# Kernel optimization log

Hardware: AMD Instinct MI355X
Metric: run time of the kernel (lower is better)

Reference implementation:

```python
import jax, jax.numpy as jnp
import numpy as np

D_IN = 512
D_OUT = 512
CONTEXT_LEN = 4096


def setup_inputs() -> dict:
    key = jax.random.key(0)
    kx, kq, kk, kv = jax.random.split(key, 4)
    x = jax.random.normal(kx, (4, 4096, D_IN), dtype=jnp.float32)
    # nn.Linear weights: shape (d_out, d_in), y = x @ W.T (no bias, qkv_bias=False)
    s = 1.0 / np.sqrt(D_IN)
    w_q = jax.random.uniform(kq, (D_OUT, D_IN), dtype=jnp.float32, minval=-s, maxval=s)
    w_k = jax.random.uniform(kk, (D_OUT, D_IN), dtype=jnp.float32, minval=-s, maxval=s)
    w_v = jax.random.uniform(kv, (D_OUT, D_IN), dtype=jnp.float32, minval=-s, maxval=s)
    return {"x": x, "w_q": w_q, "w_k": w_k, "w_v": w_v}


def reference(x, w_q, w_k, w_v):
    b, n, _ = x.shape
    q = jnp.einsum('bnd,od->bno', x, w_q)
    k = jnp.einsum('bnd,od->bno', x, w_k)
    v = jnp.einsum('bnd,od->bno', x, w_v)
    scores = jnp.einsum('bqo,bko->bqk', q, k)  # [b, n, n]
    # Faithful to source: mask buffer is triu(zeros) -> all-False, masked_fill is a no-op.
    mask = jnp.triu(jnp.zeros((CONTEXT_LEN, CONTEXT_LEN), dtype=jnp.float32), k=1).astype(bool)[:n, :n]
    scores = jnp.where(mask, -jnp.inf, scores)
    attn = jax.nn.softmax(scores / np.sqrt(D_OUT).astype(np.float32), axis=-1)
    # dropout rate 0.0 (eval/reference) -> identity
    return jnp.einsum('bqk,bko->bqo', attn, v)
```

## Files before the change

### kernel.cpp

```cpp
#include <hip/hip_runtime.h>
#include <math.h>

typedef __attribute__((ext_vector_type(8))) __bf16 bf16x8;
typedef __attribute__((ext_vector_type(8))) short  short8;
typedef __attribute__((ext_vector_type(4))) unsigned short ushort4v;
typedef __attribute__((ext_vector_type(4))) float  floatx4;

typedef __attribute__((address_space(1))) unsigned int as1_u32;
typedef __attribute__((address_space(3))) unsigned int as3_u32;

__device__ __forceinline__ void async_copy16(const void* g, void* l) {
  __builtin_amdgcn_global_load_lds((const as1_u32*)g, (as3_u32*)l, 16, 0, 0);
}

__device__ __forceinline__ unsigned short f2bf(float f) {
  union { float f; unsigned u; } v; v.f = f;
  unsigned r = v.u + 0x7fffu + ((v.u >> 16) & 1u);
  return (unsigned short)(r >> 16);
}

__device__ __forceinline__ floatx4 mfma_bf16(bf16x8 a, bf16x8 b, floatx4 c) {
  return __builtin_amdgcn_mfma_f32_16x16x32_bf16(a, b, c, 0, 0, 0);
}

__device__ __forceinline__ bf16x8 lds_frag(const unsigned short* p) {
  return *(const bf16x8*)(const void*)p;
}

__global__ __launch_bounds__(256)
void prep(const float* __restrict__ x,  const float* __restrict__ wq,
          const float* __restrict__ wk, const float* __restrict__ wv,
          unsigned short* __restrict__ Xb, unsigned short* __restrict__ Wqb,
          unsigned short* __restrict__ Wkb, unsigned short* __restrict__ Wvb) {
  const int i = blockIdx.x * 256 + threadIdx.x;
  const float* s; unsigned short* d; int off;
  if (i < 2097152)             { s = x;  d = Xb;  off = i; }
  else if (i < 2097152+65536)  { s = wq; d = Wqb; off = i - 2097152; }
  else if (i < 2097152+131072) { s = wk; d = Wkb; off = i - (2097152+65536); }
  else                         { s = wv; d = Wvb; off = i - (2097152+131072); }
  const float4 v = ((const float4*)s)[off];
  ushort4v o;
  o.x = f2bf(v.x); o.y = f2bf(v.y); o.z = f2bf(v.z); o.w = f2bf(v.w);
  *(ushort4v*)(void*)(d + (size_t)off * 4) = o;
}

__global__ __launch_bounds__(256, 2)
void gemm_qkv(const unsigned short* __restrict__ Xb,
              const unsigned short* __restrict__ Wqb,
              const unsigned short* __restrict__ Wkb,
              const unsigned short* __restrict__ Wvb,
              unsigned short* __restrict__ Q,
              unsigned short* __restrict__ K,
              unsigned short* __restrict__ Vt) {
  const int gid = blockIdx.x;
  const unsigned short *A, *B; unsigned short* C;
  int m0, n0, N;
  if (gid < 512) {
    A = Xb; B = Wqb; C = Q; N = 512;
    m0 = (gid & 127) * 128; n0 = (gid >> 7) * 128;
  } else if (gid < 1024) {
    A = Xb; B = Wkb; C = K; N = 512;
    m0 = ((gid - 512) & 127) * 128; n0 = ((gid - 512) >> 7) * 128;
  } else {
    A = Wvb; B = Xb; C = Vt; N = 16384;
    m0 = ((gid - 1024) & 3) * 128; n0 = ((gid - 1024) >> 2) * 128;
  }

  __shared__ unsigned short As[128 * 64];
  __shared__ unsigned short Bs[128 * 64];
  const int tid = threadIdx.x;
  const int w = tid >> 6, lane = tid & 63;
  const int quad = lane >> 4, l15 = lane & 15;
  const int wm = w >> 1, wn = w & 1;
  const int row_l = lane >> 3;
  const int chk   = lane & 7;
  const int s_chk = chk ^ row_l;

  floatx4 acc[16];
#pragma unroll
  for (int i = 0; i < 16; i++) acc[i] = (floatx4){0.f, 0.f, 0.f, 0.f};

  for (int kt = 0; kt < 8; kt++) {
    __syncthreads();
#pragma unroll
    for (int i = 0; i < 4; i++) {
      const int c = w * 4 + i;
      const int row = c * 8 + row_l;
      async_copy16(A + (size_t)(m0 + row) * 512 + kt * 64 + s_chk * 8, &As[c * 512]);
      async_copy16(B + (size_t)(n0 + row) * 512 + kt * 64 + s_chk * 8, &Bs[c * 512]);
    }
    __syncthreads();
#pragma unroll
    for (int kc = 0; kc < 2; kc++) {
      bf16x8 af[4], bfv[4];
#pragma unroll
      for (int i = 0; i < 4; i++) {
        const int pc = ((kc * 4 + quad) ^ (l15 & 7)) * 8;
        af[i]  = lds_frag(&As[(wm * 64 + i * 16 + l15) * 64 + pc]);
        bfv[i] = lds_frag(&Bs[(wn * 64 + i * 16 + l15) * 64 + pc]);
      }
#pragma unroll
      for (int mi = 0; mi < 4; mi++)
#pragma unroll
        for (int ni = 0; ni < 4; ni++)
          acc[mi * 4 + ni] = mfma_bf16(af[mi], bfv[ni], acc[mi * 4 + ni]);
    }
  }
#pragma unroll
  for (int mi = 0; mi < 4; mi++)
#pragma unroll
    for (int ni = 0; ni < 4; ni++)
#pragma unroll
      for (int r = 0; r < 4; r++) {
        const int row = m0 + wm * 64 + mi * 16 + quad * 4 + r;
        const int col = n0 + wn * 64 + ni * 16 + l15;
        C[(size_t)row * N + col] = f2bf(acc[mi * 4 + ni][r]);
      }
}

#define SCALE 0.044194173824159216f

__global__ __launch_bounds__(512, 2)
void attn_kernel(const unsigned short* __restrict__ Qg,
                 const unsigned short* __restrict__ Kg,
                 const unsigned short* __restrict__ Vt,
                 float* __restrict__ O) {
  __shared__ unsigned short Ks[64 * 512];
  __shared__ unsigned short Vs[512 * 64];
  __shared__ float Sx[64][65];
  __shared__ unsigned short Pb[64 * 72];
  __shared__ float m_row[64], l_row[64], a_row[64];

  const int tid = threadIdx.x;
  const int w = tid >> 6, lane = tid & 63;
  const int quad = lane >> 4, l15 = lane & 15;
  const int wq = w >> 1, wd = w & 1;

  const int g0 = blockIdx.x;
  const int g  = (g0 & 7) * 32 + (g0 >> 3);
  const int b  = g >> 6;
  const int q0 = (g & 63) * 64;

  if (tid < 64) { m_row[tid] = -3.0e38f; l_row[tid] = 0.f; }

  bf16x8 qf[16];
  {
    const unsigned short* qrow = Qg + (size_t)(b * 4096 + q0 + wq * 16 + l15) * 512;
#pragma unroll
    for (int i = 0; i < 16; i++)
      qf[i] = *(const bf16x8*)(const void*)(qrow + i * 32 + quad * 8);
  }

  floatx4 oacc[16];
#pragma unroll
  for (int i = 0; i < 16; i++) oacc[i] = (floatx4){0.f, 0.f, 0.f, 0.f};

  const unsigned short* kb0 = Kg + (size_t)b * 4096 * 512;
  const unsigned short* vb0 = Vt + (size_t)b * 4096;
  const int v_d = lane >> 3, v_schk = (lane & 7) ^ v_d;

  auto issue_K = [&](int kt_) {
#pragma unroll
    for (int u = 0; u < 8; u++) {
      const int row = w * 8 + u;
      async_copy16(kb0 + ((size_t)kt_ * 64 + row) * 512 + (lane ^ u) * 8,
                   &Ks[row * 512]);
    }
  };
  auto issue_V = [&](int kt_) {
#pragma unroll
    for (int u = 0; u < 8; u++) {
      const int d = w * 64 + u * 8 + v_d;
      async_copy16(vb0 + (size_t)kt_ * 64 + (size_t)d * 16384 + v_schk * 8,
                   &Vs[(w * 64 + u * 8) * 64]);
    }
  };

  const int srow = tid >> 3, sg = tid & 7;

  issue_K(0);

  for (int kt = 0; kt < 64; kt++) {
    asm volatile("s_waitcnt vmcnt(0)" ::: "memory");
    __builtin_amdgcn_sched_barrier(0);
    __syncthreads();
    issue_V(kt);

    floatx4 sacc[2];
    sacc[0] = (floatx4){0.f, 0.f, 0.f, 0.f};
    sacc[1] = (floatx4){0.f, 0.f, 0.f, 0.f};
#pragma unroll
    for (int kk = 0; kk < 16; kk++) {
#pragma unroll
      for (int s = 0; s < 2; s++) {
        const int krow = wd * 32 + s * 16 + l15;
        bf16x8 bfr = lds_frag(&Ks[krow * 512 + (((kk * 4 + quad) ^ (l15 & 7)) * 8)]);
        sacc[s] = mfma_bf16(qf[kk], bfr, sacc[s]);
      }
    }
#pragma unroll
    for (int s = 0; s < 2; s++)
#pragma unroll
      for (int r = 0; r < 4; r++)
        Sx[wq * 16 + quad * 4 + r][wd * 32 + s * 16 + l15] = sacc[s][r] * SCALE;
    __syncthreads();

    {
      float vals[8];
      float tmax = -3.0e38f;
#pragma unroll
      for (int j = 0; j < 8; j++) {
        float xv = Sx[srow][sg * 8 + j];
        xv = fminf(fmaxf(xv, -1.0e4f), 1.0e4f);
        vals[j] = xv;
        tmax = fmaxf(tmax, xv);
      }
      tmax = fmaxf(tmax, __shfl_xor(tmax, 1));
      tmax = fmaxf(tmax, __shfl_xor(tmax, 2));
      tmax = fmaxf(tmax, __shfl_xor(tmax, 4));
      const float m_old = m_row[srow];
      const float m_new = fmaxf(m_old, tmax);
      const float alpha = __expf(m_old - m_new);
      float lsum = 0.f;
      short8 pvec;
#pragma unroll
      for (int j = 0; j < 8; j++) {
        const float p = __expf(vals[j] - m_new);
        lsum += p;
        pvec[j] = (short)f2bf(p);
      }
      lsum += __shfl_xor(lsum, 1);
      lsum += __shfl_xor(lsum, 2);
      lsum += __shfl_xor(lsum, 4);
      *(short8*)(void*)&Pb[srow * 72 + sg * 8] = pvec;
      if (sg == 0) {
        m_row[srow] = m_new;
        l_row[srow] = l_row[srow] * alpha + lsum;
        a_row[srow] = alpha;
      }
    }
    __syncthreads();

    float ar[4];
#pragma unroll
    for (int r = 0; r < 4; r++) ar[r] = a_row[wq * 16 + quad * 4 + r];
#pragma unroll
    for (int j = 0; j < 16; j++)
#pragma unroll
      for (int r = 0; r < 4; r++) oacc[j][r] *= ar[r];
    bf16x8 pf[2];
#pragma unroll
    for (int kc = 0; kc < 2; kc++)
      pf[kc] = lds_frag(&Pb[(wq * 16 + l15) * 72 + kc * 32 + quad * 8]);

    asm volatile("s_waitcnt vmcnt(0)" ::: "memory");
    __builtin_amdgcn_sched_barrier(0);
    __syncthreads();
    if (kt < 63) issue_K(kt + 1);

#pragma unroll
    for (int j = 0; j < 16; j++) {
      const int vrow = wd * 256 + j * 16 + l15;
#pragma unroll
      for (int kc = 0; kc < 2; kc++) {
        bf16x8 bfr = lds_frag(&Vs[vrow * 64 + (((kc * 4 + quad) ^ (l15 & 7)) * 8)]);
        oacc[j] = mfma_bf16(pf[kc], bfr, oacc[j]);
      }
    }
  }

  __syncthreads();
  float invl[4];
#pragma unroll
  for (int r = 0; r < 4; r++) invl[r] = 1.0f / l_row[wq * 16 + quad * 4 + r];
#pragma unroll
  for (int j = 0; j < 16; j++) {
#pragma unroll
    for (int r = 0; r < 4; r++) {
      const int row = b * 4096 + q0 + wq * 16 + quad * 4 + r;
      O[(size_t)row * 512 + wd * 256 + j * 16 + l15] = oacc[j][r] * invl[r];
    }
  }
}

extern "C" void kernel_launch(void* const* d_in, const int* in_sizes, int n_in,
                              void* d_out, int out_size, void* d_ws, size_t ws_size,
                              hipStream_t stream) {
  const float* x   = (const float*)d_in[0];
  const float* wqf = (const float*)d_in[1];
  const float* wkf = (const float*)d_in[2];
  const float* wvf = (const float*)d_in[3];

  unsigned short* Xb  = (unsigned short*)d_out;
  unsigned short* Wqb = (unsigned short*)d_ws;
  unsigned short* Wkb = Wqb + (size_t)512 * 512;
  unsigned short* Wvb = Wkb + (size_t)512 * 512;
  unsigned short* Q   = Wvb + (size_t)512 * 512;
  unsigned short* K   = Q + (size_t)16384 * 512;
  unsigned short* Vt  = K + (size_t)16384 * 512;

  prep<<<dim3(8960), 256, 0, stream>>>(x, wqf, wkf, wvf, Xb, Wqb, Wkb, Wvb);
  gemm_qkv<<<dim3(1536), 256, 0, stream>>>(Xb, Wqb, Wkb, Wvb, Q, K, Vt);
  attn_kernel<<<dim3(256), 512, 0, stream>>>(Q, K, Vt, (float*)d_out);
}
```

Measured before the change: 350.2 us.

## Switch attention kernel to 32x32x16 MFMA with specialized QK and V-load warps

Replaces the 16x16x32 MFMA tiles in the attention kernel with 32x32x16 tiles for both QK^T and PV. Only four warps compute scores, each holding a 32-row Q slice in registers, while the other four warps issue the V async loads. PV work is remapped so each warp owns a 32-query by 128-dim output tile. The P buffer moves from padded rows to XOR-swizzled rows. The aim is fewer MFMA and LDS fragment instructions per FLOP and better operand reuse, at the cost of idle warps during QK and more Q registers per thread (32 fragments), which adds occupancy risk.

```diff
diff --git a/kernel.cpp b/kernel.cpp
--- a/kernel.cpp
+++ b/kernel.cpp
@@ -5,6 +5,7 @@
 typedef __attribute__((ext_vector_type(8))) short  short8;
 typedef __attribute__((ext_vector_type(4))) unsigned short ushort4v;
 typedef __attribute__((ext_vector_type(4))) float  floatx4;
+typedef __attribute__((ext_vector_type(16))) float floatx16;
 
 typedef __attribute__((address_space(1))) unsigned int as1_u32;
 typedef __attribute__((address_space(3))) unsigned int as3_u32;
@@ -21,6 +22,10 @@
 
 __device__ __forceinline__ floatx4 mfma_bf16(bf16x8 a, bf16x8 b, floatx4 c) {
   return __builtin_amdgcn_mfma_f32_16x16x32_bf16(a, b, c, 0, 0, 0);
+}
+
+__device__ __forceinline__ floatx16 mfma32(bf16x8 a, bf16x8 b, floatx16 c) {
+  return __builtin_amdgcn_mfma_f32_32x32x16_bf16(a, b, c, 0, 0, 0);
 }
 
 __device__ __forceinline__ bf16x8 lds_frag(const unsigned short* p) {
@@ -128,13 +133,12 @@
   __shared__ unsigned short Ks[64 * 512];
   __shared__ unsigned short Vs[512 * 64];
   __shared__ float Sx[64][65];
-  __shared__ unsigned short Pb[64 * 72];
+  __shared__ unsigned short Pb[64 * 64];
   __shared__ float m_row[64], l_row[64], a_row[64];
 
   const int tid = threadIdx.x;
   const int w = tid >> 6, lane = tid & 63;
-  const int quad = lane >> 4, l15 = lane & 15;
-  const int wq = w >> 1, wd = w & 1;
+  const int l31 = lane & 31, lh = lane >> 5, l7 = lane & 7;
 
   const int g0 = blockIdx.x;
   const int g  = (g0 & 7) * 32 + (g0 >> 3);
@@ -143,21 +147,25 @@
 
   if (tid < 64) { m_row[tid] = -3.0e38f; l_row[tid] = 0.f; }
 
-  bf16x8 qf[16];
-  {
-    const unsigned short* qrow = Qg + (size_t)(b * 4096 + q0 + wq * 16 + l15) * 512;
-#pragma unroll
-    for (int i = 0; i < 16; i++)
-      qf[i] = *(const bf16x8*)(const void*)(qrow + i * 32 + quad * 8);
-  }
-
-  floatx4 oacc[16];
-#pragma unroll
-  for (int i = 0; i < 16; i++) oacc[i] = (floatx4){0.f, 0.f, 0.f, 0.f};
+  const int wq2 = (w >> 1) & 1, wk = w & 1;
+  const int p2  = w >> 2, dbase = (w & 3) * 128;
+
+  bf16x8 qf[32];
+  if (w < 4) {
+    const unsigned short* qrow = Qg + (size_t)(b * 4096 + q0 + wq2 * 32 + l31) * 512;
+#pragma unroll
+    for (int i = 0; i < 32; i++)
+      qf[i] = *(const bf16x8*)(const void*)(qrow + i * 16 + lh * 8);
+  }
+
+  floatx16 oacc[4];
+#pragma unroll
+  for (int j = 0; j < 4; j++)
+#pragma unroll
+    for (int r = 0; r < 16; r++) oacc[j][r] = 0.f;
 
   const unsigned short* kb0 = Kg + (size_t)b * 4096 * 512;
   const unsigned short* vb0 = Vt + (size_t)b * 4096;
-  const int v_d = lane >> 3, v_schk = (lane & 7) ^ v_d;
 
   auto issue_K = [&](int kt_) {
 #pragma unroll
@@ -167,16 +175,19 @@
                    &Ks[row * 512]);
     }
   };
+  const int v_d = lane >> 3, v_schk = (lane & 7) ^ v_d;
   auto issue_V = [&](int kt_) {
 #pragma unroll
-    for (int u = 0; u < 8; u++) {
-      const int d = w * 64 + u * 8 + v_d;
+    for (int u = 0; u < 16; u++) {
+      const int unit = (w - 4) * 16 + u;
+      const int d = unit * 8 + v_d;
       async_copy16(vb0 + (size_t)kt_ * 64 + (size_t)d * 16384 + v_schk * 8,
-                   &Vs[(w * 64 + u * 8) * 64]);
+                   &Vs[unit * 512]);
     }
   };
 
   const int srow = tid >> 3, sg = tid & 7;
+  const int pb_wchunk = sg ^ (srow & 7);
 
   issue_K(0);
 
@@ -184,25 +195,24 @@
     asm volatile("s_waitcnt vmcnt(0)" ::: "memory");
     __builtin_amdgcn_sched_barrier(0);
     __syncthreads();
-    issue_V(kt);
-
-    floatx4 sacc[2];
-    sacc[0] = (floatx4){0.f, 0.f, 0.f, 0.f};
-    sacc[1] = (floatx4){0.f, 0.f, 0.f, 0.f};
-#pragma unroll
-    for (int kk = 0; kk < 16; kk++) {
-#pragma unroll
-      for (int s = 0; s < 2; s++) {
-        const int krow = wd * 32 + s * 16 + l15;
-        bf16x8 bfr = lds_frag(&Ks[krow * 512 + (((kk * 4 + quad) ^ (l15 & 7)) * 8)]);
-        sacc[s] = mfma_bf16(qf[kk], bfr, sacc[s]);
-      }
-    }
-#pragma unroll
-    for (int s = 0; s < 2; s++)
-#pragma unroll
-      for (int r = 0; r < 4; r++)
-        Sx[wq * 16 + quad * 4 + r][wd * 32 + s * 16 + l15] = sacc[s][r] * SCALE;
+    if (w >= 4) issue_V(kt);
+
+    if (w < 4) {
+      floatx16 sacc;
+#pragma unroll
+      for (int r = 0; r < 16; r++) sacc[r] = 0.f;
+      const int krow = wk * 32 + l31;
+#pragma unroll
+      for (int i = 0; i < 32; i++) {
+        bf16x8 kfr = lds_frag(&Ks[krow * 512 + (((i * 2 + lh) ^ l7) * 8)]);
+        sacc = mfma32(qf[i], kfr, sacc);
+      }
+#pragma unroll
+      for (int reg = 0; reg < 16; reg++) {
+        const int rl = (reg & 3) + 8 * (reg >> 2) + 4 * lh;
+        Sx[wq2 * 32 + rl][wk * 32 + l31] = sacc[reg] * SCALE;
+      }
+    }
     __syncthreads();
 
     {
@@ -232,7 +242,7 @@
       lsum += __shfl_xor(lsum, 1);
       lsum += __shfl_xor(lsum, 2);
       lsum += __shfl_xor(lsum, 4);
-      *(short8*)(void*)&Pb[srow * 72 + sg * 8] = pvec;
+      *(short8*)(void*)&Pb[srow * 64 + pb_wchunk * 8] = pvec;
       if (sg == 0) {
         m_row[srow] = m_new;
         l_row[srow] = l_row[srow] * alpha + lsum;
@@ -241,17 +251,19 @@
     }
     __syncthreads();
 
-    float ar[4];
-#pragma unroll
-    for (int r = 0; r < 4; r++) ar[r] = a_row[wq * 16 + quad * 4 + r];
-#pragma unroll
-    for (int j = 0; j < 16; j++)
-#pragma unroll
-      for (int r = 0; r < 4; r++) oacc[j][r] *= ar[r];
-    bf16x8 pf[2];
-#pragma unroll
-    for (int kc = 0; kc < 2; kc++)
-      pf[kc] = lds_frag(&Pb[(wq * 16 + l15) * 72 + kc * 32 + quad * 8]);
+#pragma unroll
+    for (int reg = 0; reg < 16; reg++) {
+      const float a = a_row[p2 * 32 + (reg & 3) + 8 * (reg >> 2) + 4 * lh];
+#pragma unroll
+      for (int j = 0; j < 4; j++) oacc[j][reg] *= a;
+    }
+    bf16x8 pfr[4];
+    {
+      const int q = p2 * 32 + l31;
+#pragma unroll
+      for (int kk = 0; kk < 4; kk++)
+        pfr[kk] = lds_frag(&Pb[q * 64 + (((kk * 2 + lh) ^ l7) * 8)]);
+    }
 
     asm volatile("s_waitcnt vmcnt(0)" ::: "memory");
     __builtin_amdgcn_sched_barrier(0);
@@ -259,27 +271,25 @@
     if (kt < 63) issue_K(kt + 1);
 
 #pragma unroll
-    for (int j = 0; j < 16; j++) {
-      const int vrow = wd * 256 + j * 16 + l15;
-#pragma unroll
-      for (int kc = 0; kc < 2; kc++) {
-        bf16x8 bfr = lds_frag(&Vs[vrow * 64 + (((kc * 4 + quad) ^ (l15 & 7)) * 8)]);
-        oacc[j] = mfma_bf16(pf[kc], bfr, oacc[j]);
+    for (int j = 0; j < 4; j++) {
+      const int d = dbase + j * 32 + l31;
+#pragma unroll
+      for (int kk = 0; kk < 4; kk++) {
+        bf16x8 vfr = lds_frag(&Vs[d * 64 + (((kk * 2 + lh) ^ l7) * 8)]);
+        oacc[j] = mfma32(pfr[kk], vfr, oacc[j]);
       }
     }
   }
 
   __syncthreads();
-  float invl[4];
-#pragma unroll
-  for (int r = 0; r < 4; r++) invl[r] = 1.0f / l_row[wq * 16 + quad * 4 + r];
-#pragma unroll
-  for (int j = 0; j < 16; j++) {
-#pragma unroll
-    for (int r = 0; r < 4; r++) {
-      const int row = b * 4096 + q0 + wq * 16 + quad * 4 + r;
-      O[(size_t)row * 512 + wd * 256 + j * 16 + l15] = oacc[j][r] * invl[r];
-    }
+#pragma unroll
+  for (int reg = 0; reg < 16; reg++) {
+    const int rl = (reg & 3) + 8 * (reg >> 2) + 4 * lh;
+    const float inv = 1.0f / l_row[p2 * 32 + rl];
+    const int row = b * 4096 + q0 + p2 * 32 + rl;
+#pragma unroll
+    for (int j = 0; j < 4; j++)
+      O[(size_t)row * 512 + dbase + j * 32 + l31] = oacc[j][reg] * inv;
   }
 }
 
```

After: 642.3 us. 1.83x slower.

## Halve attention query/key tiles to 32 and use 4-wave blocks for more CTAs

Applied to the files above, without the earlier changes.

Attention blocks shrink from 64 queries with 8 waves to 32 queries with 4 waves, and each key step now covers 32 keys instead of 64. The grid grows from 256 to 512 blocks, so all CUs on the device get work, and LDS per block roughly halves. The P and V tiles get new XOR swizzles, and the QK^T product splits into two accumulators to give more MFMA independence. In exchange there are twice as many loop iterations, each with three barriers and a softmax pass, and K/V are reloaded per 32-query block, which doubles global K/V traffic.

```diff
diff --git a/kernel.cpp b/kernel.cpp
--- a/kernel.cpp
+++ b/kernel.cpp
@@ -3,6 +3,7 @@
 
 typedef __attribute__((ext_vector_type(8))) __bf16 bf16x8;
 typedef __attribute__((ext_vector_type(8))) short  short8;
+typedef __attribute__((ext_vector_type(4))) short  short4v;
 typedef __attribute__((ext_vector_type(4))) unsigned short ushort4v;
 typedef __attribute__((ext_vector_type(4))) float  floatx4;
 
@@ -120,28 +121,29 @@
 
 #define SCALE 0.044194173824159216f
 
-__global__ __launch_bounds__(512, 2)
+__global__ __launch_bounds__(256, 2)
 void attn_kernel(const unsigned short* __restrict__ Qg,
                  const unsigned short* __restrict__ Kg,
                  const unsigned short* __restrict__ Vt,
                  float* __restrict__ O) {
-  __shared__ unsigned short Ks[64 * 512];
-  __shared__ unsigned short Vs[512 * 64];
-  __shared__ float Sx[64][65];
-  __shared__ unsigned short Pb[64 * 72];
-  __shared__ float m_row[64], l_row[64], a_row[64];
+  __shared__ unsigned short Ks[32 * 512];
+  __shared__ unsigned short Vs[512 * 32];
+  __shared__ float Sx[32][33];
+  __shared__ unsigned short Pb[32 * 32];
+  __shared__ float m_row[32], l_row[32], a_row[32];
 
   const int tid = threadIdx.x;
   const int w = tid >> 6, lane = tid & 63;
   const int quad = lane >> 4, l15 = lane & 15;
-  const int wq = w >> 1, wd = w & 1;
 
   const int g0 = blockIdx.x;
-  const int g  = (g0 & 7) * 32 + (g0 >> 3);
-  const int b  = g >> 6;
-  const int q0 = (g & 63) * 64;
-
-  if (tid < 64) { m_row[tid] = -3.0e38f; l_row[tid] = 0.f; }
+  const int g  = (g0 & 7) * 64 + (g0 >> 3);
+  const int b  = g >> 7;
+  const int q0 = (g & 127) * 32;
+
+  if (tid < 32) { m_row[tid] = -3.0e38f; l_row[tid] = 0.f; }
+
+  const int wq = w >> 1, wk = w & 1;
 
   bf16x8 qf[16];
   {
@@ -153,64 +155,66 @@
 
   floatx4 oacc[16];
 #pragma unroll
-  for (int i = 0; i < 16; i++) oacc[i] = (floatx4){0.f, 0.f, 0.f, 0.f};
+  for (int t = 0; t < 16; t++) oacc[t] = (floatx4){0.f, 0.f, 0.f, 0.f};
 
   const unsigned short* kb0 = Kg + (size_t)b * 4096 * 512;
   const unsigned short* vb0 = Vt + (size_t)b * 4096;
-  const int v_d = lane >> 3, v_schk = (lane & 7) ^ v_d;
 
   auto issue_K = [&](int kt_) {
 #pragma unroll
     for (int u = 0; u < 8; u++) {
       const int row = w * 8 + u;
-      async_copy16(kb0 + ((size_t)kt_ * 64 + row) * 512 + (lane ^ u) * 8,
+      async_copy16(kb0 + ((size_t)kt_ * 32 + row) * 512 + (lane ^ u) * 8,
                    &Ks[row * 512]);
     }
   };
+  const int v_d4 = lane >> 2;
+  const int v_sc = (lane & 3) ^ (v_d4 & 3);
   auto issue_V = [&](int kt_) {
 #pragma unroll
     for (int u = 0; u < 8; u++) {
-      const int d = w * 64 + u * 8 + v_d;
-      async_copy16(vb0 + (size_t)kt_ * 64 + (size_t)d * 16384 + v_schk * 8,
-                   &Vs[(w * 64 + u * 8) * 64]);
+      const int unit = w * 8 + u;
+      const int d = unit * 16 + v_d4;
+      async_copy16(vb0 + (size_t)kt_ * 32 + (size_t)d * 16384 + v_sc * 8,
+                   &Vs[unit * 512]);
     }
   };
 
   const int srow = tid >> 3, sg = tid & 7;
+  const int pb_w8 = (((sg >> 1) ^ (srow & 3)) << 1) | (sg & 1);
 
   issue_K(0);
 
-  for (int kt = 0; kt < 64; kt++) {
+  for (int kt = 0; kt < 128; kt++) {
     asm volatile("s_waitcnt vmcnt(0)" ::: "memory");
     __builtin_amdgcn_sched_barrier(0);
     __syncthreads();
     issue_V(kt);
 
-    floatx4 sacc[2];
-    sacc[0] = (floatx4){0.f, 0.f, 0.f, 0.f};
-    sacc[1] = (floatx4){0.f, 0.f, 0.f, 0.f};
-#pragma unroll
-    for (int kk = 0; kk < 16; kk++) {
-#pragma unroll
-      for (int s = 0; s < 2; s++) {
-        const int krow = wd * 32 + s * 16 + l15;
-        bf16x8 bfr = lds_frag(&Ks[krow * 512 + (((kk * 4 + quad) ^ (l15 & 7)) * 8)]);
-        sacc[s] = mfma_bf16(qf[kk], bfr, sacc[s]);
-      }
-    }
-#pragma unroll
-    for (int s = 0; s < 2; s++)
+    {
+      floatx4 sa = (floatx4){0.f, 0.f, 0.f, 0.f};
+      floatx4 sb = (floatx4){0.f, 0.f, 0.f, 0.f};
+      const int krow = wk * 16 + l15;
+      const int ksw = krow & 7;
+#pragma unroll
+      for (int i = 0; i < 16; i += 2) {
+        bf16x8 k0 = lds_frag(&Ks[krow * 512 + (((i * 4 + quad) ^ ksw) * 8)]);
+        sa = mfma_bf16(qf[i], k0, sa);
+        bf16x8 k1 = lds_frag(&Ks[krow * 512 + ((((i + 1) * 4 + quad) ^ ksw) * 8)]);
+        sb = mfma_bf16(qf[i + 1], k1, sb);
+      }
 #pragma unroll
       for (int r = 0; r < 4; r++)
-        Sx[wq * 16 + quad * 4 + r][wd * 32 + s * 16 + l15] = sacc[s][r] * SCALE;
+        Sx[wq * 16 + quad * 4 + r][wk * 16 + l15] = (sa[r] + sb[r]) * SCALE;
+    }
     __syncthreads();
 
     {
-      float vals[8];
+      float vals[4];
       float tmax = -3.0e38f;
 #pragma unroll
-      for (int j = 0; j < 8; j++) {
-        float xv = Sx[srow][sg * 8 + j];
+      for (int j = 0; j < 4; j++) {
+        float xv = Sx[srow][sg * 4 + j];
         xv = fminf(fmaxf(xv, -1.0e4f), 1.0e4f);
         vals[j] = xv;
         tmax = fmaxf(tmax, xv);
@@ -222,9 +226,9 @@
       const float m_new = fmaxf(m_old, tmax);
       const float alpha = __expf(m_old - m_new);
       float lsum = 0.f;
-      short8 pvec;
-#pragma unroll
-      for (int j = 0; j < 8; j++) {
+      short4v pvec;
+#pragma unroll
+      for (int j = 0; j < 4; j++) {
         const float p = __expf(vals[j] - m_new);
         lsum += p;
         pvec[j] = (short)f2bf(p);
@@ -232,7 +236,7 @@
       lsum += __shfl_xor(lsum, 1);
       lsum += __shfl_xor(lsum, 2);
       lsum += __shfl_xor(lsum, 4);
-      *(short8*)(void*)&Pb[srow * 72 + sg * 8] = pvec;
+      *(short4v*)(void*)&Pb[srow * 32 + pb_w8 * 4] = pvec;
       if (sg == 0) {
         m_row[srow] = m_new;
         l_row[srow] = l_row[srow] * alpha + lsum;
@@ -241,44 +245,49 @@
     }
     __syncthreads();
 
-    float ar[4];
-#pragma unroll
-    for (int r = 0; r < 4; r++) ar[r] = a_row[wq * 16 + quad * 4 + r];
-#pragma unroll
-    for (int j = 0; j < 16; j++)
-#pragma unroll
-      for (int r = 0; r < 4; r++) oacc[j][r] *= ar[r];
-    bf16x8 pf[2];
-#pragma unroll
-    for (int kc = 0; kc < 2; kc++)
-      pf[kc] = lds_frag(&Pb[(wq * 16 + l15) * 72 + kc * 32 + quad * 8]);
+    float ar[2][4];
+#pragma unroll
+    for (int qt = 0; qt < 2; qt++)
+#pragma unroll
+      for (int r = 0; r < 4; r++) ar[qt][r] = a_row[qt * 16 + quad * 4 + r];
+#pragma unroll
+    for (int t = 0; t < 16; t++)
+#pragma unroll
+      for (int r = 0; r < 4; r++) oacc[t][r] *= ar[t >> 3][r];
+    bf16x8 pfr[2];
+#pragma unroll
+    for (int qt = 0; qt < 2; qt++) {
+      const int q = qt * 16 + l15;
+      pfr[qt] = lds_frag(&Pb[q * 32 + ((quad ^ (l15 & 3)) * 8)]);
+    }
 
     asm volatile("s_waitcnt vmcnt(0)" ::: "memory");
     __builtin_amdgcn_sched_barrier(0);
     __syncthreads();
-    if (kt < 63) issue_K(kt + 1);
-
-#pragma unroll
-    for (int j = 0; j < 16; j++) {
-      const int vrow = wd * 256 + j * 16 + l15;
-#pragma unroll
-      for (int kc = 0; kc < 2; kc++) {
-        bf16x8 bfr = lds_frag(&Vs[vrow * 64 + (((kc * 4 + quad) ^ (l15 & 7)) * 8)]);
-        oacc[j] = mfma_bf16(pf[kc], bfr, oacc[j]);
-      }
+    if (kt < 127) issue_K(kt + 1);
+
+#pragma unroll
+    for (int t = 0; t < 16; t++) {
+      const int qt = t >> 3, dt = t & 7;
+      const int d = w * 128 + dt * 16 + l15;
+      bf16x8 vfr = lds_frag(&Vs[d * 32 + ((quad ^ (l15 & 3)) * 8)]);
+      oacc[t] = mfma_bf16(pfr[qt], vfr, oacc[t]);
     }
   }
 
   __syncthreads();
-  float invl[4];
-#pragma unroll
-  for (int r = 0; r < 4; r++) invl[r] = 1.0f / l_row[wq * 16 + quad * 4 + r];
-#pragma unroll
-  for (int j = 0; j < 16; j++) {
+  float invl[2][4];
+#pragma unroll
+  for (int qt = 0; qt < 2; qt++)
+#pragma unroll
+    for (int r = 0; r < 4; r++) invl[qt][r] = 1.0f / l_row[qt * 16 + quad * 4 + r];
+#pragma unroll
+  for (int t = 0; t < 16; t++) {
+    const int qt = t >> 3, dt = t & 7;
 #pragma unroll
     for (int r = 0; r < 4; r++) {
-      const int row = b * 4096 + q0 + wq * 16 + quad * 4 + r;
-      O[(size_t)row * 512 + wd * 256 + j * 16 + l15] = oacc[j][r] * invl[r];
+      const int row = b * 4096 + q0 + qt * 16 + quad * 4 + r;
+      O[(size_t)row * 512 + w * 128 + dt * 16 + l15] = oacc[t][r] * invl[qt][r];
     }
   }
 }
@@ -301,5 +310,5 @@
 
   prep<<<dim3(8960), 256, 0, stream>>>(x, wqf, wkf, wvf, Xb, Wqb, Wkb, Wvb);
   gemm_qkv<<<dim3(1536), 256, 0, stream>>>(Xb, Wqb, Wkb, Wvb, Q, K, Vt);
-  attn_kernel<<<dim3(256), 512, 0, stream>>>(Q, K, Vt, (float*)d_out);
-}
+  attn_kernel<<<dim3(512), 256, 0, stream>>>(Q, K, Vt, (float*)d_out);
+}
```

Result: slower. 386.3 us (+10.3%).
